# Kernel optimization log

Measured on AMD Instinct MI355X. Metric: run time of the kernel, lower is better.

Reference implementation:

```python
import jax, jax.numpy as jnp
import numpy as np

B, L, E = 4, 1024, 1024
H, D = 16, 64          # num_heads, head_dim
HID = H * D            # hidden_dim == 1024
R = 4                  # nrels


def setup_inputs() -> dict:
    key = jax.random.key(0)
    ks = jax.random.split(key, 8)
    query = jax.random.normal(ks[0], (B, L, E), dtype=jnp.float32)
    rels = jax.random.uniform(ks[1], (B, L, L, R), dtype=jnp.float32)
    attn_mask = jax.random.normal(ks[2], (B, L, L), dtype=jnp.float32)
    key_padding_mask = jax.random.bernoulli(ks[3], 0.9, (B, L, L))
    # xavier-ish init for linear weights
    proj_w = jax.random.normal(ks[4], (4 * HID, E), dtype=jnp.float32) * (2.0 / (4 * HID + E)) ** 0.5
    proj_b = jnp.zeros((4 * HID,), dtype=jnp.float32)
    out_w = jax.random.normal(ks[5], (E, HID), dtype=jnp.float32) * (2.0 / (E + HID)) ** 0.5
    out_b = jnp.zeros((E,), dtype=jnp.float32)
    rels_bias = jax.random.uniform(ks[6], (R, H), dtype=jnp.float32, minval=-0.1, maxval=0.1)
    return {"query": query, "rels": rels, "attn_mask": attn_mask,
            "key_padding_mask": key_padding_mask, "proj_w": proj_w, "proj_b": proj_b,
            "out_w": out_w, "out_b": out_b, "rels_bias": rels_bias}


def reference(query, rels, attn_mask, key_padding_mask, proj_w, proj_b, out_w, out_b, rels_bias):
    b, l, _ = query.shape
    # fused QKVG projection
    qkvg = query @ proj_w.T + proj_b                       # [b, l, 4*HID]
    q, k, v, g = jnp.split(qkvg, 4, axis=-1)
    q = q.reshape(b, l, H, D)
    k = k.reshape(b, l, H, D)
    v = v.reshape(b, l, H, D)
    g = g.reshape(b, l, H, D)
    scores = jnp.einsum('bihd,bjhd->bijh', q, k)
    scores = scores + jnp.einsum('bijr,rh->bijh', rels, rels_bias)
    scores = scores * (D ** -0.5)
    # NOTE: log_softmax over the HEADS axis (dim=-1), as in the source,
    # then additive log-domain mask over keys, then exp.
    w = jnp.exp(jax.nn.log_softmax(scores, axis=-1) + attn_mask[:, :, :, None])
    w = jnp.where(key_padding_mask[:, :, :, None], w, 0.0)
    attn_out = jnp.einsum('bijh,bjhd->bihd', w, jnp.tanh(v))
    gated = attn_out * jax.nn.sigmoid(g)                   # [b, l, H, D]
    out = gated.reshape(b, l, HID) @ out_w.T + out_b       # [b, l, E]
    return (out, w)
```

## Files before the change

kernel.cpp:

```cpp
#include <hip/hip_runtime.h>

typedef unsigned short u16;
using bf16x8 = __attribute__((ext_vector_type(8))) short;
using f32x4  = __attribute__((ext_vector_type(4))) float;

__device__ __forceinline__ u16 f2bf(float f) {
  unsigned u = __builtin_bit_cast(unsigned, f);
  u += 0x7fffu + ((u >> 16) & 1u);
  return (u16)(u >> 16);
}
__device__ __forceinline__ float bf2f(u16 h) {
  unsigned u = ((unsigned)h) << 16;
  return __builtin_bit_cast(float, u);
}
__device__ __forceinline__ float f16f(unsigned bits) {
  return (float)__builtin_bit_cast(_Float16, (unsigned short)(bits & 0xffffu));
}
__device__ __forceinline__ u16 f2h(float f) {
  _Float16 h = (_Float16)f;
  return __builtin_bit_cast(unsigned short, h);
}
__device__ __forceinline__ float fast_rcp(float x){ return __builtin_amdgcn_rcpf(x); }
__device__ __forceinline__ float tanh_fast(float x){
  float ax = fabsf(x);
  float e = __expf(-2.f*ax);
  float t = (1.f - e) * fast_rcp(1.f + e);
  return copysignf(t, x);
}
__device__ __forceinline__ float sigmoid_fast(float x){
  return fast_rcp(1.f + __expf(-x));
}

__device__ __forceinline__ int kperm(int k) {
  return (k & ~63) | ((k & 15) << 2) | ((k >> 4) & 3);
}

__global__ __launch_bounds__(256) void cvt_bf16(const float* __restrict__ src,
                                                u16* __restrict__ dst, int n){
  int i = (blockIdx.x * 256 + threadIdx.x) * 8;
  if (i >= n) return;
  float4 a = *(const float4*)(src + i);
  float4 b = *(const float4*)(src + i + 4);
  uint4 u;
  u.x = (unsigned)f2bf(a.x) | ((unsigned)f2bf(a.y) << 16);
  u.y = (unsigned)f2bf(a.z) | ((unsigned)f2bf(a.w) << 16);
  u.z = (unsigned)f2bf(b.x) | ((unsigned)f2bf(b.y) << 16);
  u.w = (unsigned)f2bf(b.z) | ((unsigned)f2bf(b.w) << 16);
  *(uint4*)(dst + i) = u;
}

__global__ __launch_bounds__(256) void cvt_owb_perm(const float* __restrict__ src,
                                                    u16* __restrict__ dst){
  const int t = blockIdx.x * 256 + threadIdx.x;
  const int n = t >> 8;
  const int g = t & 255;
  const int h = g >> 4;
  const int c = g & 15;
  const float* s = src + n*1024 + h*64 + c;
  uint2 o;
  o.x = (unsigned)f2bf(s[0])  | ((unsigned)f2bf(s[16]) << 16);
  o.y = (unsigned)f2bf(s[32]) | ((unsigned)f2bf(s[48]) << 16);
  *(uint2*)(dst + n*1024 + g*4) = o;
}

template<int EPI>
__global__ __launch_bounds__(256, 2) void gemm_bt(
    const u16* __restrict__ A, const u16* __restrict__ B, const float* __restrict__ bias,
    u16* __restrict__ oq, u16* __restrict__ ok, u16* __restrict__ ov, u16* __restrict__ og,
    float* __restrict__ outp, int K)
{
  __shared__ u16 a_lds[4*128*8];
  __shared__ u16 b_lds[4*128*8];
  const int tid  = threadIdx.x;
  const int lane = tid & 63;
  const int wv   = tid >> 6;
  const int wr   = wv >> 1, wc = wv & 1;
  const int col  = lane & 15, quad = lane >> 4;
  const int m0   = blockIdx.y * 128, n0 = blockIdx.x * 128;
  f32x4 acc[4][4] = {};
  for (int k0 = 0; k0 < K; k0 += 32) {
    __syncthreads();
    #pragma unroll
    for (int s = 0; s < 2; s++) {
      int cid = tid + 256*s;
      int row = cid >> 2, qk = cid & 3;
      *(bf16x8*)(&a_lds[(qk*128+row)*8]) = *(const bf16x8*)(A + (m0+row)*K + k0 + qk*8);
      *(bf16x8*)(&b_lds[(qk*128+row)*8]) = *(const bf16x8*)(B + (n0+row)*K + k0 + qk*8);
    }
    __syncthreads();
    bf16x8 af[4], bfr[4];
    #pragma unroll
    for (int mi=0;mi<4;mi++) af[mi]  = *(const bf16x8*)(&a_lds[(quad*128 + wr*64 + mi*16 + col)*8]);
    #pragma unroll
    for (int ni=0;ni<4;ni++) bfr[ni] = *(const bf16x8*)(&b_lds[(quad*128 + wc*64 + ni*16 + col)*8]);
    #pragma unroll
    for (int mi=0;mi<4;mi++)
      #pragma unroll
      for (int ni=0;ni<4;ni++)
        acc[mi][ni] = __builtin_amdgcn_mfma_f32_16x16x32_bf16(af[mi], bfr[ni], acc[mi][ni], 0, 0, 0);
  }
  #pragma unroll
  for (int mi=0;mi<4;mi++) {
    #pragma unroll
    for (int ni=0;ni<4;ni++) {
      #pragma unroll
      for (int r=0;r<4;r++) {
        const int m = m0 + wr*64 + mi*16 + quad*4 + r;
        const int n = n0 + wc*64 + ni*16 + col;
        const float val = acc[mi][ni][r] + bias[n];
        if (EPI == 0) {
          const int idx = m*1024 + (n & 1023);
          const int quarter = n0 >> 10;
          if (quarter == 0)      oq[idx] = f2bf(val);
          else if (quarter == 1) ok[idx] = f2bf(val);
          else if (quarter == 2) ov[idx] = f2bf(tanh_fast(val));
          else {
            og[m*1024 + kperm(n & 1023)] = f2bf(sigmoid_fast(val));
          }
        } else {
          outp[m*1024 + n] = val;
        }
      }
    }
  }
}

__global__ __launch_bounds__(256) void vtrans(const u16* __restrict__ vin, u16* __restrict__ vout){
  __shared__ u16 tile[64][68];
  const int bh = blockIdx.y;
  const int b = bh >> 4, h = bh & 15;
  const int i0 = blockIdx.x * 64;
  const int t = threadIdx.x;
  #pragma unroll
  for (int s=0;s<4;s++){
    int idx = t + 256*s;
    int ti = idx >> 4;
    int d4 = (idx & 15) * 4;
    uint2 v = *(const uint2*)(vin + ((size_t)((b*1024 + i0 + ti)*16 + h))*64 + d4);
    tile[ti][d4+0] = (u16)(v.x);
    tile[ti][d4+1] = (u16)(v.x >> 16);
    tile[ti][d4+2] = (u16)(v.y);
    tile[ti][d4+3] = (u16)(v.y >> 16);
  }
  __syncthreads();
  #pragma unroll
  for (int s=0;s<4;s++){
    int idx = t + 256*s;
    int d  = idx >> 4;
    int t4 = (idx & 15) * 4;
    uint2 o;
    o.x = (unsigned)tile[t4+0][d] | ((unsigned)tile[t4+1][d] << 16);
    o.y = (unsigned)tile[t4+2][d] | ((unsigned)tile[t4+3][d] << 16);
    *(uint2*)(vout + ((size_t)((b*16 + h)*64 + d))*1024 + i0 + t4) = o;
  }
}

__global__ __launch_bounds__(256, 3) void attn_kernel(
    const u16* __restrict__ qb, const u16* __restrict__ kb,
    const u16* __restrict__ vt,
    const float* __restrict__ rels, const float* __restrict__ amask,
    const int* __restrict__ kpm, const float* __restrict__ rbias,
    float* __restrict__ wout,
    u16* __restrict__ o0, u16* __restrict__ o1, u16* __restrict__ o2)
{
  __shared__ u16 w_lds[16*16*72];
  __shared__ float stageF[4][1024];
  const int bid = blockIdx.x;
  const int b  = (bid >> 1) & 3;
  const int it = (bid & 1) | ((bid >> 3) << 1);
  const int i0 = it << 4;
  const int js = blockIdx.y;
  const int t0 = js*5 + (js > 0);
  const int t1 = t0 + (js == 0 ? 6 : 5);
  const int tid = threadIdx.x;
  const int lane = tid & 63;
  const int wv  = tid >> 6;
  const int col = lane & 15, quad = lane >> 4;

  float rbv[4][16];
  #pragma unroll
  for (int r=0;r<4;r++)
    #pragma unroll
    for (int h=0;h<16;h++)
      rbv[r][h] = rbias[r*16+h];

  f32x4 Oa[4][4] = {};

  for (int t = t0; t < t1; t++) {
    const int j0b = t << 6;
    const int j0  = j0b + (wv << 4);
    float4 rl4[4]; float mk4[4]; int pd4[4];
    #pragma unroll
    for (int r=0; r<4; r++) {
      const int pij = (b*1024 + i0 + quad*4 + r)*1024 + j0 + col;
      rl4[r] = *(const float4*)(rels + (size_t)pij*4);
      mk4[r] = amask[pij];
      pd4[r] = kpm[pij];
    }
    f32x4 sc[16] = {};
    #pragma unroll
    for (int h=0; h<16; h++) {
      #pragma unroll
      for (int c=0; c<2; c++) {
        bf16x8 aq = *(const bf16x8*)(qb + (size_t)(b*1024 + i0 + col)*1024 + h*64 + c*32 + quad*8);
        bf16x8 bk = *(const bf16x8*)(kb + (size_t)(b*1024 + j0 + col)*1024 + h*64 + c*32 + quad*8);
        sc[h] = __builtin_amdgcn_mfma_f32_16x16x32_bf16(aq, bk, sc[h], 0, 0, 0);
      }
    }
    #pragma unroll
    for (int r=0; r<4; r++) {
      const float4 rl = rl4[r];
      float p[16];
      float mx = -1e30f;
      #pragma unroll
      for (int h=0;h<16;h++) {
        float s = sc[h][r];
        s = fmaf(rl.x, rbv[0][h], s);
        s = fmaf(rl.y, rbv[1][h], s);
        s = fmaf(rl.z, rbv[2][h], s);
        s = fmaf(rl.w, rbv[3][h], s);
        s *= 0.125f;
        p[h] = s;
        mx = fmaxf(mx, s);
      }
      float S = 0.f;
      #pragma unroll
      for (int h=0;h<16;h++) { p[h] = __expf(p[h] - mx); S += p[h]; }
      const float scl = pd4[r] ? (__expf(mk4[r]) * fast_rcp(S)) : 0.f;
      #pragma unroll
      for (int h=0;h<16;h++) p[h] *= scl;
      #pragma unroll
      for (int hg=0; hg<4; hg++) {
        const int ph = hg ^ ((col + quad) & 3);
        f32x4 v4 = { p[4*hg+0], p[4*hg+1], p[4*hg+2], p[4*hg+3] };
        *(f32x4*)&stageF[wv][quad*256 + col*16 + ph*4] = v4;
      }
      #pragma unroll
      for (int h=0;h<16;h++)
        w_lds[(h*16 + quad*4 + r)*72 + (wv<<4) + col] = f2bf(p[h]);
      asm volatile("s_waitcnt lgkmcnt(0)" ::: "memory");
      const int rcol = lane >> 2, rhg = lane & 3;
      #pragma unroll
      for (int qt=0; qt<4; qt++) {
        const int ph = rhg ^ ((rcol + qt) & 3);
        f32x4 w4 = *(const f32x4*)&stageF[wv][qt*256 + rcol*16 + ph*4];
        float* dst = wout + ((size_t)((b*1024 + i0 + qt*4 + r)*1024 + j0b + (wv<<4)))*16 + lane*4;
        __builtin_nontemporal_store(w4, (f32x4*)dst);
      }
    }
    __syncthreads();
    #pragma unroll
    for (int hh=0; hh<4; hh++) {
      const int h = (wv<<2) + hh;
      #pragma unroll
      for (int c2=0; c2<2; c2++) {
        bf16x8 aw = *(const bf16x8*)(&w_lds[(h*16 + col)*72 + c2*32 + quad*8]);
        #pragma unroll
        for (int dt=0; dt<4; dt++) {
          bf16x8 bv = *(const bf16x8*)(vt + (size_t)((b*16 + h)*64 + dt*16 + col)*1024 + j0b + c2*32 + quad*8);
          Oa[hh][dt] = __builtin_amdgcn_mfma_f32_16x16x32_bf16(aw, bv, Oa[hh][dt], 0, 0, 0);
        }
      }
    }
    __syncthreads();
  }
  u16* op = (js == 0) ? o0 : ((js == 1) ? o1 : o2);
  #pragma unroll
  for (int hh=0; hh<4; hh++) {
    const int h = (wv<<2) + hh;
    #pragma unroll
    for (int r=0; r<4; r++) {
      const int i = i0 + quad*4 + r;
      uint2 pk;
      pk.x = (unsigned)f2h(Oa[hh][0][r]) | ((unsigned)f2h(Oa[hh][1][r]) << 16);
      pk.y = (unsigned)f2h(Oa[hh][2][r]) | ((unsigned)f2h(Oa[hh][3][r]) << 16);
      *(uint2*)(op + ((size_t)((b*1024 + i)*16 + h))*64 + col*4) = pk;
    }
  }
}

__global__ __launch_bounds__(256) void reduce_gate(
    const u16* o0, const u16* __restrict__ o1, const u16* __restrict__ o2,
    const u16* __restrict__ sg, u16* gated)
{
  const int i = (blockIdx.x * 256 + threadIdx.x) * 8;
  uint4 a = *(const uint4*)(o0 + i);
  uint4 b = *(const uint4*)(o1 + i);
  uint4 c = *(const uint4*)(o2 + i);
  uint4 s = *(const uint4*)(sg + i);
  const unsigned* ap = (const unsigned*)&a;
  const unsigned* bp = (const unsigned*)&b;
  const unsigned* cp = (const unsigned*)&c;
  const unsigned* sp = (const unsigned*)&s;
  uint4 r;
  unsigned* rp = (unsigned*)&r;
  #pragma unroll
  for (int k=0;k<4;k++){
    float f0 = f16f(ap[k]) + f16f(bp[k]) + f16f(cp[k]);
    float f1 = f16f(ap[k]>>16) + f16f(bp[k]>>16) + f16f(cp[k]>>16);
    f0 *= bf2f((u16)(sp[k] & 0xffffu));
    f1 *= bf2f((u16)(sp[k] >> 16));
    rp[k] = (unsigned)f2bf(f0) | ((unsigned)f2bf(f1) << 16);
  }
  *(uint4*)(gated + i) = r;
}

extern "C" void kernel_launch(void* const* d_in, const int* in_sizes, int n_in,
                              void* d_out, int out_size, void* d_ws, size_t ws_size,
                              hipStream_t stream) {
  const float* query  = (const float*)d_in[0];
  const float* rels   = (const float*)d_in[1];
  const float* amask  = (const float*)d_in[2];
  const int*   kpm    = (const int*)d_in[3];
  const float* proj_w = (const float*)d_in[4];
  const float* proj_b = (const float*)d_in[5];
  const float* out_w  = (const float*)d_in[6];
  const float* out_b  = (const float*)d_in[7];
  const float* rbias  = (const float*)d_in[8];

  float* out  = (float*)d_out;
  float* wout = out + (size_t)4*1024*1024;

  char* ws = (char*)d_ws;
  u16* q_b   = (u16*)(ws + ((size_t) 0 << 20));
  u16* k_b   = (u16*)(ws + ((size_t) 8 << 20));
  u16* sg_b  = (u16*)(ws + ((size_t)16 << 20));
  u16* vth   = (u16*)(ws + ((size_t)24 << 20));
  u16* vt    = (u16*)(ws + ((size_t)32 << 20));
  u16* qryb  = (u16*)(ws + ((size_t)40 << 20));
  u16* pwb   = (u16*)(ws + ((size_t)48 << 20));
  u16* owb   = (u16*)(ws + ((size_t)56 << 20));
  u16* o0 = qryb;
  u16* o1 = pwb;
  u16* o2 = vth;
  u16* gated = o0;

  cvt_bf16<<<2048, 256, 0, stream>>>(query,  qryb, 4*1024*1024);
  cvt_bf16<<<2048, 256, 0, stream>>>(proj_w, pwb,  4*1024*1024);
  cvt_owb_perm<<<1024, 256, 0, stream>>>(out_w, owb);

  gemm_bt<0><<<dim3(32,32), 256, 0, stream>>>(qryb, pwb, proj_b,
                                              q_b, k_b, vth, sg_b, nullptr, 1024);
  vtrans<<<dim3(16,64), 256, 0, stream>>>(vth, vt);
  attn_kernel<<<dim3(256,3), 256, 0, stream>>>(q_b, k_b, vt,
                                               rels, amask, kpm, rbias, wout,
                                               o0, o1, o2);
  reduce_gate<<<2048, 256, 0, stream>>>(o0, o1, o2, sg_b, gated);
  gemm_bt<1><<<dim3(8,32), 256, 0, stream>>>(gated, owb, out_b,
                                             nullptr, nullptr, nullptr, nullptr, out, 1024);
}
```

Measured before the change: 703.9 us.

## Split attention keys four ways, shrink LDS staging, prefetch masks, use direct-to-LDS loads

```diff
diff --git a/kernel.cpp b/kernel.cpp
--- a/kernel.cpp
+++ b/kernel.cpp
@@ -29,6 +29,11 @@
 }
 __device__ __forceinline__ float sigmoid_fast(float x){
   return fast_rcp(1.f + __expf(-x));
+}
+__device__ __forceinline__ void gload_lds16(const u16* g, u16* l) {
+  __builtin_amdgcn_global_load_lds(
+      (const __attribute__((address_space(1))) unsigned*)g,
+      (__attribute__((address_space(3))) unsigned*)l, 16, 0, 0);
 }
 
 __device__ __forceinline__ int kperm(int k) {
@@ -82,10 +87,10 @@
     __syncthreads();
     #pragma unroll
     for (int s = 0; s < 2; s++) {
-      int cid = tid + 256*s;
-      int row = cid >> 2, qk = cid & 3;
-      *(bf16x8*)(&a_lds[(qk*128+row)*8]) = *(const bf16x8*)(A + (m0+row)*K + k0 + qk*8);
-      *(bf16x8*)(&b_lds[(qk*128+row)*8]) = *(const bf16x8*)(B + (n0+row)*K + k0 + qk*8);
+      const int cid = s*256 + tid;
+      const int row = cid & 127, qk = cid >> 7;
+      gload_lds16(A + (size_t)(m0+row)*K + k0 + qk*8, &a_lds[cid*8]);
+      gload_lds16(B + (size_t)(n0+row)*K + k0 + qk*8, &b_lds[cid*8]);
     }
     __syncthreads();
     bf16x8 af[4], bfr[4];
@@ -155,23 +160,24 @@
   }
 }
 
-__global__ __launch_bounds__(256, 3) void attn_kernel(
+__global__ __launch_bounds__(256, 4) void attn_kernel(
     const u16* __restrict__ qb, const u16* __restrict__ kb,
     const u16* __restrict__ vt,
     const float* __restrict__ rels, const float* __restrict__ amask,
     const int* __restrict__ kpm, const float* __restrict__ rbias,
     float* __restrict__ wout,
-    u16* __restrict__ o0, u16* __restrict__ o1, u16* __restrict__ o2)
+    u16* __restrict__ o0, u16* __restrict__ o1,
+    u16* __restrict__ o2, u16* __restrict__ o3)
 {
   __shared__ u16 w_lds[16*16*72];
-  __shared__ float stageF[4][1024];
+  __shared__ float stg[4][256];
   const int bid = blockIdx.x;
   const int b  = (bid >> 1) & 3;
   const int it = (bid & 1) | ((bid >> 3) << 1);
   const int i0 = it << 4;
   const int js = blockIdx.y;
-  const int t0 = js*5 + (js > 0);
-  const int t1 = t0 + (js == 0 ? 6 : 5);
+  const int t0 = js << 2;
+  const int t1 = t0 + 4;
   const int tid = threadIdx.x;
   const int lane = tid & 63;
   const int wv  = tid >> 6;
@@ -186,10 +192,9 @@
 
   f32x4 Oa[4][4] = {};
 
-  for (int t = t0; t < t1; t++) {
-    const int j0b = t << 6;
-    const int j0  = j0b + (wv << 4);
-    float4 rl4[4]; float mk4[4]; int pd4[4];
+  float4 rl4[4]; float mk4[4]; int pd4[4];
+  {
+    const int j0 = (t0 << 6) + (wv << 4);
     #pragma unroll
     for (int r=0; r<4; r++) {
       const int pij = (b*1024 + i0 + quad*4 + r)*1024 + j0 + col;
@@ -197,6 +202,11 @@
       mk4[r] = amask[pij];
       pd4[r] = kpm[pij];
     }
+  }
+
+  for (int t = t0; t < t1; t++) {
+    const int j0b = t << 6;
+    const int j0  = j0b + (wv << 4);
     f32x4 sc[16] = {};
     #pragma unroll
     for (int h=0; h<16; h++) {
@@ -230,25 +240,37 @@
       #pragma unroll
       for (int h=0;h<16;h++) p[h] *= scl;
       #pragma unroll
-      for (int hg=0; hg<4; hg++) {
-        const int ph = hg ^ ((col + quad) & 3);
-        f32x4 v4 = { p[4*hg+0], p[4*hg+1], p[4*hg+2], p[4*hg+3] };
-        *(f32x4*)&stageF[wv][quad*256 + col*16 + ph*4] = v4;
-      }
-      #pragma unroll
       for (int h=0;h<16;h++)
         w_lds[(h*16 + quad*4 + r)*72 + (wv<<4) + col] = f2bf(p[h]);
-      asm volatile("s_waitcnt lgkmcnt(0)" ::: "memory");
-      const int rcol = lane >> 2, rhg = lane & 3;
-      #pragma unroll
-      for (int qt=0; qt<4; qt++) {
-        const int ph = rhg ^ ((rcol + qt) & 3);
-        f32x4 w4 = *(const f32x4*)&stageF[wv][qt*256 + rcol*16 + ph*4];
-        float* dst = wout + ((size_t)((b*1024 + i0 + qt*4 + r)*1024 + j0b + (wv<<4)))*16 + lane*4;
+      #pragma unroll
+      for (int u=0; u<4; u++) {
+        if (quad == u) {
+          #pragma unroll
+          for (int hg=0; hg<4; hg++) {
+            const int ph = hg ^ ((col + (col>>2)) & 3);
+            f32x4 v4 = { p[4*hg+0], p[4*hg+1], p[4*hg+2], p[4*hg+3] };
+            *(f32x4*)&stg[wv][col*16 + ph*4] = v4;
+          }
+        }
+        asm volatile("s_waitcnt lgkmcnt(0)" ::: "memory");
+        const int cr = lane >> 2, hr = lane & 3;
+        const int pr = hr ^ ((cr + (cr>>2)) & 3);
+        f32x4 w4 = *(const f32x4*)&stg[wv][cr*16 + pr*4];
+        float* dst = wout + ((size_t)((b*1024 + i0 + u*4 + r)*1024 + j0b + (wv<<4)))*16 + lane*4;
         __builtin_nontemporal_store(w4, (f32x4*)dst);
       }
     }
     __syncthreads();
+    if (t+1 < t1) {
+      const int j0n = ((t+1) << 6) + (wv << 4);
+      #pragma unroll
+      for (int r=0; r<4; r++) {
+        const int pij = (b*1024 + i0 + quad*4 + r)*1024 + j0n + col;
+        rl4[r] = *(const float4*)(rels + (size_t)pij*4);
+        mk4[r] = amask[pij];
+        pd4[r] = kpm[pij];
+      }
+    }
     #pragma unroll
     for (int hh=0; hh<4; hh++) {
       const int h = (wv<<2) + hh;
@@ -264,7 +286,7 @@
     }
     __syncthreads();
   }
-  u16* op = (js == 0) ? o0 : ((js == 1) ? o1 : o2);
+  u16* op = (js == 0) ? o0 : ((js == 1) ? o1 : ((js == 2) ? o2 : o3));
   #pragma unroll
   for (int hh=0; hh<4; hh++) {
     const int h = (wv<<2) + hh;
@@ -281,23 +303,26 @@
 
 __global__ __launch_bounds__(256) void reduce_gate(
     const u16* o0, const u16* __restrict__ o1, const u16* __restrict__ o2,
+    const u16* __restrict__ o3,
     const u16* __restrict__ sg, u16* gated)
 {
   const int i = (blockIdx.x * 256 + threadIdx.x) * 8;
   uint4 a = *(const uint4*)(o0 + i);
   uint4 b = *(const uint4*)(o1 + i);
   uint4 c = *(const uint4*)(o2 + i);
+  uint4 d = *(const uint4*)(o3 + i);
   uint4 s = *(const uint4*)(sg + i);
   const unsigned* ap = (const unsigned*)&a;
   const unsigned* bp = (const unsigned*)&b;
   const unsigned* cp = (const unsigned*)&c;
+  const unsigned* dp = (const unsigned*)&d;
   const unsigned* sp = (const unsigned*)&s;
   uint4 r;
   unsigned* rp = (unsigned*)&r;
   #pragma unroll
   for (int k=0;k<4;k++){
-    float f0 = f16f(ap[k]) + f16f(bp[k]) + f16f(cp[k]);
-    float f1 = f16f(ap[k]>>16) + f16f(bp[k]>>16) + f16f(cp[k]>>16);
+    float f0 = (f16f(ap[k])     + f16f(bp[k]))     + (f16f(cp[k])     + f16f(dp[k]));
+    float f1 = (f16f(ap[k]>>16) + f16f(bp[k]>>16)) + (f16f(cp[k]>>16) + f16f(dp[k]>>16));
     f0 *= bf2f((u16)(sp[k] & 0xffffu));
     f1 *= bf2f((u16)(sp[k] >> 16));
     rp[k] = (unsigned)f2bf(f0) | ((unsigned)f2bf(f1) << 16);
@@ -333,6 +358,7 @@
   u16* o0 = qryb;
   u16* o1 = pwb;
   u16* o2 = vth;
+  u16* o3 = (u16*)out;
   u16* gated = o0;
 
   cvt_bf16<<<2048, 256, 0, stream>>>(query,  qryb, 4*1024*1024);
@@ -342,10 +368,10 @@
   gemm_bt<0><<<dim3(32,32), 256, 0, stream>>>(qryb, pwb, proj_b,
                                               q_b, k_b, vth, sg_b, nullptr, 1024);
   vtrans<<<dim3(16,64), 256, 0, stream>>>(vth, vt);
-  attn_kernel<<<dim3(256,3), 256, 0, stream>>>(q_b, k_b, vt,
+  attn_kernel<<<dim3(256,4), 256, 0, stream>>>(q_b, k_b, vt,
                                                rels, amask, kpm, rbias, wout,
-                                               o0, o1, o2);
-  reduce_gate<<<2048, 256, 0, stream>>>(o0, o1, o2, sg_b, gated);
+                                               o0, o1, o2, o3);
+  reduce_gate<<<2048, 256, 0, stream>>>(o0, o1, o2, o3, sg_b, gated);
   gemm_bt<1><<<dim3(8,32), 256, 0, stream>>>(gated, owb, out_b,
                                              nullptr, nullptr, nullptr, nullptr, out, 1024);
 }
```

Result: slower. 913.9 us (+29.8%).
